# Optimization experiments

Measured on AMD Instinct MI355X. Metric: run time of the kernel, lower is better.

## Reference

```python
import jax, jax.numpy as jnp
import numpy as np

B, N, C, W = 64, 4096, 128, 64
WIN = N - W + 1  # 4033, length of each sliding-filter input
BN_EPS = 1e-5


def setup_inputs() -> dict:
    key = jax.random.key(0)
    ks = jax.random.split(key, 8)
    s_in = 1.0 / np.sqrt(WIN)   # nn.Linear default init scale
    s_2 = 1.0 / np.sqrt(2.0)
    s_out = 1.0 / np.sqrt(W)
    return {
        "x": jax.random.normal(ks[0], (B, N, C, 2), dtype=jnp.float32),
        "w_in_real": jax.random.normal(ks[1], (C, WIN), dtype=jnp.float32) * s_in,
        "w_in_imag": jax.random.normal(ks[2], (C, WIN), dtype=jnp.float32) * s_in,
        "A_nonlin": jax.random.normal(ks[3], (C, 2, 2), dtype=jnp.float32) * s_2,
        "Wc": jax.random.normal(ks[4], (2, 2), dtype=jnp.float32) * s_2,
        "w_out_real": jax.random.normal(ks[5], (C, W), dtype=jnp.float32) * s_out,
        "w_out_imag": jax.random.normal(ks[6], (C, W), dtype=jnp.float32) * s_out,
        "bn_gamma": jnp.ones((C,), dtype=jnp.float32),
        "bn_beta": jnp.zeros((C,), dtype=jnp.float32),
    }


def _depthwise_corr(sig, w):
    # sig: [B, N, C], w: [C, K] -> [B, N-K+1, C]
    # filtered[b, t, c] = sum_k sig[b, t+k, c] * w[c, k]  (matches per-channel Linear on slices)
    rhs = w.T[:, None, :]  # [K, 1, C]
    return jax.lax.conv_general_dilated(
        sig, rhs, window_strides=(1,), padding="VALID",
        dimension_numbers=("NWC", "WIO", "NWC"),
        feature_group_count=sig.shape[-1])


def reference(x, w_in_real, w_in_imag, A_nonlin, Wc, w_out_real, w_out_imag, bn_gamma, bn_beta):
    xr, xi = x[..., 0], x[..., 1]               # [B, N, C]
    # --- per-channel sliding input filters (out_window positions) ---
    fr = _depthwise_corr(xr, w_in_real)          # [B, W, C]
    fi = _depthwise_corr(xi, w_in_imag)          # [B, W, C]
    v = jnp.stack([fr, fi], axis=-1)             # [B, W, C, 2]
    # --- per-channel 2x2 linear: out_j = sum_i A[c, j, i] * v_i ---
    u = jnp.einsum("bwci,cji->bwcj", v, A_nonlin)
    amp = jnp.sum(u * u, axis=-1, keepdims=True)  # r^2 + i^2
    u = amp * u
    # --- shared 2x2 coeff linear ---
    u = jnp.einsum("bwci,ji->bwcj", u, Wc)
    # --- per-channel output filters over the out_window axis ---
    out_r = jnp.einsum("bwc,cw->bc", u[..., 0], w_out_real)
    out_i = jnp.einsum("bwc,cw->bc", u[..., 1], w_out_imag)
    out = jnp.stack([out_r, out_i], axis=-1)     # [B, C, 2]
    # --- BatchNorm1d(C), training-mode batch statistics over (B, last) dims ---
    mean = jnp.mean(out, axis=(0, 2), keepdims=True)
    var = jnp.mean((out - mean) ** 2, axis=(0, 2), keepdims=True)
    out = (out - mean) * jax.lax.rsqrt(var + BN_EPS)
    return out * bn_gamma[None, :, None] + bn_beta[None, :, None]
```

## Files before the change

kernel.cpp:

```cpp
#include <hip/hip_runtime.h>

typedef float v2f __attribute__((ext_vector_type(2)));
typedef float v4f __attribute__((ext_vector_type(4)));

#define B_ 64
#define N_ 4096
#define C_ 128
#define W_ 64
#define WIN_ 4033
#define CG 16
#define NCHUNK 256
#define KPAD 4176
#define WSTRIDE 338

__global__ void prep_w(const float* __restrict__ wr, const float* __restrict__ wi,
                       v2f* __restrict__ w2pad) {
  int idx = blockIdx.x * 256 + threadIdx.x;
  int c = idx / KPAD;
  int kk = idx - c * KPAD;
  int k = kk - 64;
  v2f v = {0.f, 0.f};
  if (k >= 0 && k < WIN_) {
    v.x = wr[c * WIN_ + k];
    v.y = wi[c * WIN_ + k];
  }
  w2pad[idx] = v;
}

__global__ __launch_bounds__(256, 2) void conv_main(
    const v2f* __restrict__ x2,
    const v2f* __restrict__ w2pad,
    const float* __restrict__ Anl,
    const float* __restrict__ Wcm,
    const float* __restrict__ wor,
    const float* __restrict__ woi,
    float* __restrict__ pre) {
  __shared__ __attribute__((aligned(16))) v2f wsh[CG * WSTRIDE];

  int tid = threadIdx.x;
  int bb = blockIdx.x >> 3;
  int cg = blockIdx.x & 7;
  int cbase = cg * CG;
  int cl = (tid >> 2) & 15;
  int t0g = tid & 3;
  int np = tid >> 6;
  int t0 = t0g << 4;
  int nbase = np << 6;

  v2f zero = {0.f, 0.f};
  v2f acc[16];
#pragma unroll
  for (int i = 0; i < 16; i++) acc[i] = zero;

  const v2f* xg = x2 + (size_t)bb * N_ * C_ + cbase + cl;
  const v2f* wrow = wsh + cl * WSTRIDE;

  for (int n0 = 0; n0 < N_; n0 += NCHUNK) {
    {
      const v4f* wsrc = (const v4f*)(w2pad + (size_t)cbase * KPAD + n0);
      v4f* wdst = (v4f*)wsh;
      for (int i = tid; i < CG * 168; i += 256) {
        int c = i / 168;
        int u = i - c * 168;
        wdst[c * 169 + u] = wsrc[(size_t)c * (KPAD / 2) + u];
      }
    }
    __syncthreads();

    v2f wA[16], wB[16], xA[16], xB[16];
#pragma unroll
    for (int m = 0; m < 16; m++) wA[m] = wrow[nbase + 48 - t0 + m];
#pragma unroll
    for (int j = 0; j < 16; j++) xA[j] = xg[(size_t)(n0 + nbase + j) * C_];

    auto pref = [&](int nb, v2f* xv) {
#pragma unroll
      for (int j = 0; j < 16; j++) xv[j] = xg[(size_t)(n0 + nb + j) * C_];
    };
    auto do16 = [&](int nb, const v2f* xv, const v2f* wold, v2f* wnew) {
#pragma unroll
      for (int j = 0; j < 16; j++) wnew[j] = wrow[nb + 64 - t0 + j];
#pragma unroll
      for (int j = 0; j < 16; j++) {
#pragma unroll
        for (int i = 0; i < 16; i++) {
          int e = j - i;
          v2f wv = (e < 0) ? wold[16 + e] : wnew[e];
          acc[i] = __builtin_elementwise_fma(xv[j], wv, acc[i]);
        }
      }
    };

    pref(nbase + 16, xB);
    do16(nbase + 0, xA, wA, wB);
    pref(nbase + 32, xA);
    do16(nbase + 16, xB, wB, wA);
    pref(nbase + 48, xB);
    do16(nbase + 32, xA, wA, wB);
    do16(nbase + 48, xB, wB, wA);
    __syncthreads();
  }

  v2f* fpart = wsh;
#pragma unroll
  for (int i = 0; i < 16; i++) fpart[((np * CG + cl) << 6) + t0 + i] = acc[i];
  __syncthreads();

  int cl2 = tid & 15;
  int tq = tid >> 4;
  int c = cbase + cl2;
  float a00 = Anl[c * 4 + 0], a01 = Anl[c * 4 + 1];
  float a10 = Anl[c * 4 + 2], a11 = Anl[c * 4 + 3];
  float wc00 = Wcm[0], wc01 = Wcm[1], wc10 = Wcm[2], wc11 = Wcm[3];
  float or_ = 0.f, oi_ = 0.f;
#pragma unroll
  for (int q = 0; q < 4; q++) {
    int t = tq + (q << 4);
    v2f f = fpart[(0 * CG + cl2) * 64 + t] + fpart[(1 * CG + cl2) * 64 + t] +
            fpart[(2 * CG + cl2) * 64 + t] + fpart[(3 * CG + cl2) * 64 + t];
    float ur = a00 * f.x + a01 * f.y;
    float ui = a10 * f.x + a11 * f.y;
    float amp = ur * ur + ui * ui;
    ur *= amp;
    ui *= amp;
    float vr = wc00 * ur + wc01 * ui;
    float vi = wc10 * ur + wc11 * ui;
    or_ += vr * wor[c * 64 + t];
    oi_ += vi * woi[c * 64 + t];
  }
  or_ += __shfl_down(or_, 16, 64);
  oi_ += __shfl_down(oi_, 16, 64);
  or_ += __shfl_down(or_, 32, 64);
  oi_ += __shfl_down(oi_, 32, 64);
  __syncthreads();
  v2f* opart = wsh;
  if ((tid & 63) < 16) {
    v2f t = {or_, oi_};
    opart[(tid >> 6) * 16 + cl2] = t;
  }
  __syncthreads();
  if (tid < 16) {
    v2f r = opart[cl2] + opart[16 + cl2] + opart[32 + cl2] + opart[48 + cl2];
    pre[((size_t)bb * C_ + cbase + cl2) * 2 + 0] = r.x;
    pre[((size_t)bb * C_ + cbase + cl2) * 2 + 1] = r.y;
  }
}

__global__ void bn_kernel(const float* __restrict__ pre, const float* __restrict__ gamma,
                          const float* __restrict__ beta, float* __restrict__ out) {
  int c = blockIdx.x, tid = threadIdx.x;
  int b = tid >> 1, comp = tid & 1;
  float v = pre[((size_t)b * C_ + c) * 2 + comp];
  float s = v, s2 = v * v;
#pragma unroll
  for (int d = 32; d > 0; d >>= 1) {
    s += __shfl_down(s, d, 64);
    s2 += __shfl_down(s2, d, 64);
  }
  __shared__ float red[4];
  if ((tid & 63) == 0) {
    red[(tid >> 6) * 2 + 0] = s;
    red[(tid >> 6) * 2 + 1] = s2;
  }
  __syncthreads();
  float sum = red[0] + red[2], sumsq = red[1] + red[3];
  float mean = sum * 0.0078125f;
  float var = sumsq * 0.0078125f - mean * mean;
  float inv = rsqrtf(var + 1e-5f);
  out[((size_t)b * C_ + c) * 2 + comp] = (v - mean) * inv * gamma[c] + beta[c];
}

extern "C" void kernel_launch(void* const* d_in, const int* in_sizes, int n_in,
                              void* d_out, int out_size, void* d_ws, size_t ws_size,
                              hipStream_t stream) {
  (void)in_sizes; (void)n_in; (void)out_size; (void)ws_size;
  const float* x   = (const float*)d_in[0];
  const float* wir = (const float*)d_in[1];
  const float* wii = (const float*)d_in[2];
  const float* Anl = (const float*)d_in[3];
  const float* Wcm = (const float*)d_in[4];
  const float* wrr = (const float*)d_in[5];
  const float* wri = (const float*)d_in[6];
  const float* gam = (const float*)d_in[7];
  const float* bet = (const float*)d_in[8];

  v2f* w2pad = (v2f*)d_ws;
  float* pre = (float*)((char*)d_ws + (size_t)C_ * KPAD * sizeof(v2f));

  prep_w<<<(C_ * KPAD) / 256, 256, 0, stream>>>(wir, wii, w2pad);
  conv_main<<<B_ * (C_ / CG), 256, 0, stream>>>((const v2f*)x, w2pad, Anl, Wcm,
                                                wrr, wri, pre);
  bn_kernel<<<C_, 128, 0, stream>>>(pre, gam, bet, (float*)d_out);
}
```

Measured before the change: 495.1 us.

## Split sequence across blocks with atomic reduction, larger register tiles, inline weight staging

Reworks the sliding-filter kernel. Each thread now holds 32 output positions instead of 16 and uses a register window that shifts by 8, so each shared-memory weight load feeds more FMAs. Each block covers two batches, and the sequence is split into two halves handled by separate blocks whose partial sums are combined with global atomics into a zeroed buffer. The padded-weight prep kernel is removed and weights are staged straight from the inputs into skewed shared memory to avoid bank conflicts. The nonlinearity and output filter move into their own kernel. The cost is a memset, many atomics, an extra launch, and higher register pressure from the 32-accumulator tile.

New measurement: 936.6 us. 89.2% more time.

```diff
diff --git a/kernel.cpp b/kernel.cpp
--- a/kernel.cpp
+++ b/kernel.cpp
@@ -1,7 +1,6 @@
 #include <hip/hip_runtime.h>
 
 typedef float v2f __attribute__((ext_vector_type(2)));
-typedef float v4f __attribute__((ext_vector_type(4)));
 
 #define B_ 64
 #define N_ 4096
@@ -9,140 +8,153 @@
 #define W_ 64
 #define WIN_ 4033
 #define CG 16
-#define NCHUNK 256
-#define KPAD 4176
-#define WSTRIDE 338
-
-__global__ void prep_w(const float* __restrict__ wr, const float* __restrict__ wi,
-                       v2f* __restrict__ w2pad) {
-  int idx = blockIdx.x * 256 + threadIdx.x;
-  int c = idx / KPAD;
-  int kk = idx - c * KPAD;
-  int k = kk - 64;
-  v2f v = {0.f, 0.f};
-  if (k >= 0 && k < WIN_) {
-    v.x = wr[c * WIN_ + k];
-    v.y = wi[c * WIN_ + k];
-  }
-  w2pad[idx] = v;
-}
+#define CHUNK 256
+#define STAGE 336
+#define SROW 357
+#define NH 2
+#define HALF_N 2048
+
+__device__ __forceinline__ int skew(int u) { return u + (u >> 4); }
 
 __global__ __launch_bounds__(256, 2) void conv_main(
     const v2f* __restrict__ x2,
-    const v2f* __restrict__ w2pad,
-    const float* __restrict__ Anl,
-    const float* __restrict__ Wcm,
-    const float* __restrict__ wor,
-    const float* __restrict__ woi,
-    float* __restrict__ pre) {
-  __shared__ __attribute__((aligned(16))) v2f wsh[CG * WSTRIDE];
+    const float* __restrict__ wr,
+    const float* __restrict__ wi,
+    float* __restrict__ facc) {
+  __shared__ __attribute__((aligned(16))) v2f wsh[CG * SROW];
 
   int tid = threadIdx.x;
-  int bb = blockIdx.x >> 3;
-  int cg = blockIdx.x & 7;
+  int bid = blockIdx.x;
+  int half = bid & 1;
+  int cg = (bid >> 1) & 7;
+  int bp = bid >> 4;
+  int cl = tid & 15;
+  int tg = (tid >> 4) & 1;
+  int np = (tid >> 5) & 3;
+  int bsel = tid >> 7;
+  int b = bp * 2 + bsel;
   int cbase = cg * CG;
-  int cl = (tid >> 2) & 15;
-  int t0g = tid & 3;
-  int np = tid >> 6;
-  int t0 = t0g << 4;
-  int nbase = np << 6;
-
-  v2f zero = {0.f, 0.f};
-  v2f acc[16];
-#pragma unroll
-  for (int i = 0; i < 16; i++) acc[i] = zero;
-
-  const v2f* xg = x2 + (size_t)bb * N_ * C_ + cbase + cl;
-  const v2f* wrow = wsh + cl * WSTRIDE;
-
-  for (int n0 = 0; n0 < N_; n0 += NCHUNK) {
-    {
-      const v4f* wsrc = (const v4f*)(w2pad + (size_t)cbase * KPAD + n0);
-      v4f* wdst = (v4f*)wsh;
-      for (int i = tid; i < CG * 168; i += 256) {
-        int c = i / 168;
-        int u = i - c * 168;
-        wdst[c * 169 + u] = wsrc[(size_t)c * (KPAD / 2) + u];
+  int c = cbase + cl;
+  int t0 = tg * 32;
+  int halfstart = half * HALF_N;
+  int nthr = np * 64;
+
+  v2f acc[32];
+#pragma unroll
+  for (int i = 0; i < 32; i++) acc[i] = (v2f){0.f, 0.f};
+
+  const v2f* xg = x2 + ((size_t)b * N_ + halfstart) * C_ + c;
+  const v2f* wrow = wsh + cl * SROW;
+
+  v2f win[40];
+  v2f xw[3][8];
+
+  for (int ch = 0; ch < 8; ++ch) {
+    int n0 = halfstart + ch * CHUNK;
+    int ncb = ch * CHUNK + nthr;
+
+#pragma unroll
+    for (int j = 0; j < 8; j++) xw[0][j] = xg[(size_t)(ncb + j) * C_];
+#pragma unroll
+    for (int j = 0; j < 8; j++) xw[1][j] = xg[(size_t)(ncb + 8 + j) * C_];
+
+    __syncthreads();
+
+#pragma unroll
+    for (int cc = 0; cc < CG; ++cc) {
+      const float* wrp = wr + (size_t)(cbase + cc) * WIN_;
+      const float* wip = wi + (size_t)(cbase + cc) * WIN_;
+      {
+        int u = tid;
+        int k = n0 + u - 64;
+        bool ok = (unsigned)k < (unsigned)WIN_;
+        v2f v;
+        v.x = ok ? wrp[k] : 0.f;
+        v.y = ok ? wip[k] : 0.f;
+        wsh[cc * SROW + skew(u)] = v;
+      }
+      if (tid < STAGE - 256) {
+        int u = tid + 256;
+        int k = n0 + u - 64;
+        bool ok = (unsigned)k < (unsigned)WIN_;
+        v2f v;
+        v.x = ok ? wrp[k] : 0.f;
+        v.y = ok ? wip[k] : 0.f;
+        wsh[cc * SROW + skew(u)] = v;
       }
     }
     __syncthreads();
 
-    v2f wA[16], wB[16], xA[16], xB[16];
-#pragma unroll
-    for (int m = 0; m < 16; m++) wA[m] = wrow[nbase + 48 - t0 + m];
-#pragma unroll
-    for (int j = 0; j < 16; j++) xA[j] = xg[(size_t)(n0 + nbase + j) * C_];
-
-    auto pref = [&](int nb, v2f* xv) {
-#pragma unroll
-      for (int j = 0; j < 16; j++) xv[j] = xg[(size_t)(n0 + nb + j) * C_];
-    };
-    auto do16 = [&](int nb, const v2f* xv, const v2f* wold, v2f* wnew) {
-#pragma unroll
-      for (int j = 0; j < 16; j++) wnew[j] = wrow[nb + 64 - t0 + j];
-#pragma unroll
-      for (int j = 0; j < 16; j++) {
-#pragma unroll
-        for (int i = 0; i < 16; i++) {
-          int e = j - i;
-          v2f wv = (e < 0) ? wold[16 + e] : wnew[e];
-          acc[i] = __builtin_elementwise_fma(xv[j], wv, acc[i]);
+#pragma unroll
+    for (int m = 0; m < 40; m++) win[m] = wrow[skew(nthr + 33 - t0 + m)];
+
+#pragma unroll
+    for (int blk = 0; blk < 8; ++blk) {
+      int nbc = nthr + blk * 8;
+      if (blk < 6) {
+#pragma unroll
+        for (int j = 0; j < 8; j++)
+          xw[(blk + 2) % 3][j] = xg[(size_t)(ch * CHUNK + nbc + 16 + j) * C_];
+      }
+      const v2f* xv = xw[blk % 3];
+#pragma unroll
+      for (int j = 0; j < 8; j++) {
+#pragma unroll
+        for (int i = 0; i < 32; i++) {
+          acc[i] = __builtin_elementwise_fma(xv[j], win[31 + j - i], acc[i]);
         }
       }
-    };
-
-    pref(nbase + 16, xB);
-    do16(nbase + 0, xA, wA, wB);
-    pref(nbase + 32, xA);
-    do16(nbase + 16, xB, wB, wA);
-    pref(nbase + 48, xB);
-    do16(nbase + 32, xA, wA, wB);
-    do16(nbase + 48, xB, wB, wA);
-    __syncthreads();
-  }
-
-  v2f* fpart = wsh;
-#pragma unroll
-  for (int i = 0; i < 16; i++) fpart[((np * CG + cl) << 6) + t0 + i] = acc[i];
-  __syncthreads();
-
-  int cl2 = tid & 15;
-  int tq = tid >> 4;
-  int c = cbase + cl2;
+      if (blk < 7) {
+#pragma unroll
+        for (int m = 0; m < 32; m++) win[m] = win[m + 8];
+#pragma unroll
+        for (int r = 0; r < 8; r++)
+          win[32 + r] = wrow[skew(nbc + 73 - t0 + r)];
+      }
+    }
+  }
+
+  float* fp = facc + (((size_t)b * C_ + c) * 64 + t0) * 2;
+#pragma unroll
+  for (int i = 0; i < 32; i++) {
+    atomicAdd(fp + 2 * i + 0, acc[i].x);
+    atomicAdd(fp + 2 * i + 1, acc[i].y);
+  }
+}
+
+__global__ void nonlin_out(const float* __restrict__ faccf,
+                           const float* __restrict__ Anl,
+                           const float* __restrict__ Wcm,
+                           const float* __restrict__ wor,
+                           const float* __restrict__ woi,
+                           float* __restrict__ pre) {
+  int tid = threadIdx.x;
+  int p = tid >> 6;
+  int t = tid & 63;
+  int idx = blockIdx.x * 4 + p;
+  int b = idx >> 7;
+  int c = idx & 127;
+  const v2f* f2 = (const v2f*)faccf;
+  v2f f = f2[((size_t)b * C_ + c) * 64 + t];
   float a00 = Anl[c * 4 + 0], a01 = Anl[c * 4 + 1];
   float a10 = Anl[c * 4 + 2], a11 = Anl[c * 4 + 3];
-  float wc00 = Wcm[0], wc01 = Wcm[1], wc10 = Wcm[2], wc11 = Wcm[3];
-  float or_ = 0.f, oi_ = 0.f;
-#pragma unroll
-  for (int q = 0; q < 4; q++) {
-    int t = tq + (q << 4);
-    v2f f = fpart[(0 * CG + cl2) * 64 + t] + fpart[(1 * CG + cl2) * 64 + t] +
-            fpart[(2 * CG + cl2) * 64 + t] + fpart[(3 * CG + cl2) * 64 + t];
-    float ur = a00 * f.x + a01 * f.y;
-    float ui = a10 * f.x + a11 * f.y;
-    float amp = ur * ur + ui * ui;
-    ur *= amp;
-    ui *= amp;
-    float vr = wc00 * ur + wc01 * ui;
-    float vi = wc10 * ur + wc11 * ui;
-    or_ += vr * wor[c * 64 + t];
-    oi_ += vi * woi[c * 64 + t];
-  }
-  or_ += __shfl_down(or_, 16, 64);
-  oi_ += __shfl_down(oi_, 16, 64);
-  or_ += __shfl_down(or_, 32, 64);
-  oi_ += __shfl_down(oi_, 32, 64);
-  __syncthreads();
-  v2f* opart = wsh;
-  if ((tid & 63) < 16) {
-    v2f t = {or_, oi_};
-    opart[(tid >> 6) * 16 + cl2] = t;
-  }
-  __syncthreads();
-  if (tid < 16) {
-    v2f r = opart[cl2] + opart[16 + cl2] + opart[32 + cl2] + opart[48 + cl2];
-    pre[((size_t)bb * C_ + cbase + cl2) * 2 + 0] = r.x;
-    pre[((size_t)bb * C_ + cbase + cl2) * 2 + 1] = r.y;
+  float ur = a00 * f.x + a01 * f.y;
+  float ui = a10 * f.x + a11 * f.y;
+  float amp = ur * ur + ui * ui;
+  ur *= amp;
+  ui *= amp;
+  float vr = Wcm[0] * ur + Wcm[1] * ui;
+  float vi = Wcm[2] * ur + Wcm[3] * ui;
+  float or_ = vr * wor[c * 64 + t];
+  float oi_ = vi * woi[c * 64 + t];
+#pragma unroll
+  for (int d = 32; d > 0; d >>= 1) {
+    or_ += __shfl_down(or_, d, 64);
+    oi_ += __shfl_down(oi_, d, 64);
+  }
+  if (t == 0) {
+    pre[((size_t)b * C_ + c) * 2 + 0] = or_;
+    pre[((size_t)b * C_ + c) * 2 + 1] = oi_;
   }
 }
 
@@ -184,11 +196,11 @@
   const float* gam = (const float*)d_in[7];
   const float* bet = (const float*)d_in[8];
 
-  v2f* w2pad = (v2f*)d_ws;
-  float* pre = (float*)((char*)d_ws + (size_t)C_ * KPAD * sizeof(v2f));
-
-  prep_w<<<(C_ * KPAD) / 256, 256, 0, stream>>>(wir, wii, w2pad);
-  conv_main<<<B_ * (C_ / CG), 256, 0, stream>>>((const v2f*)x, w2pad, Anl, Wcm,
-                                                wrr, wri, pre);
+  float* facc = (float*)d_ws;
+  float* pre  = facc + (size_t)B_ * C_ * 64 * 2;
+
+  hipMemsetAsync(facc, 0, (size_t)B_ * C_ * 64 * 2 * sizeof(float), stream);
+  conv_main<<<32 * 8 * NH, 256, 0, stream>>>((const v2f*)x, wir, wii, facc);
+  nonlin_out<<<(B_ * C_) / 4, 256, 0, stream>>>(facc, Anl, Wcm, wrr, wri, pre);
   bn_kernel<<<C_, 128, 0, stream>>>(pre, gam, bet, (float*)d_out);
 }
```

## Shrink per-thread tile to 8x8, halve channel group, use packed FMA asm

Applied to the files above, without the earlier changes.

The conv kernel is restructured so each thread computes 8 output positions over 8-sample input blocks with a sliding 16-entry weight register window, instead of 16x16 tiles. Channel groups shrink from 16 to 8, which doubles the grid, and launch bounds rise to 4 blocks per CU to cut register pressure and raise occupancy. The x loads for the next chunk are issued before the weight staging sync, and the FMAs use inline v_pk_fma_f32. The cost is less register reuse per x/w load, more LDS traffic per FMA, and scalar (non-vector) weight staging copies.

Measured after the change: 550.3 us. +11.2%, slower.

```diff
diff --git a/kernel.cpp b/kernel.cpp
--- a/kernel.cpp
+++ b/kernel.cpp
@@ -1,17 +1,23 @@
 #include <hip/hip_runtime.h>
 
 typedef float v2f __attribute__((ext_vector_type(2)));
-typedef float v4f __attribute__((ext_vector_type(4)));
 
 #define B_ 64
 #define N_ 4096
 #define C_ 128
 #define W_ 64
 #define WIN_ 4033
-#define CG 16
-#define NCHUNK 256
+#define CG 8
+#define CHUNK 256
+#define STAGE 336
+#define SROW 337
 #define KPAD 4176
-#define WSTRIDE 338
+
+__device__ __forceinline__ v2f pk_fma(v2f a, v2f b, v2f c) {
+  v2f d;
+  asm("v_pk_fma_f32 %0, %1, %2, %3" : "=v"(d) : "v"(a), "v"(b), "v"(c));
+  return d;
+}
 
 __global__ void prep_w(const float* __restrict__ wr, const float* __restrict__ wi,
                        v2f* __restrict__ w2pad) {
@@ -27,7 +33,7 @@
   w2pad[idx] = v;
 }
 
-__global__ __launch_bounds__(256, 2) void conv_main(
+__global__ __launch_bounds__(256, 4) void conv_main(
     const v2f* __restrict__ x2,
     const v2f* __restrict__ w2pad,
     const float* __restrict__ Anl,
@@ -35,89 +41,87 @@
     const float* __restrict__ wor,
     const float* __restrict__ woi,
     float* __restrict__ pre) {
-  __shared__ __attribute__((aligned(16))) v2f wsh[CG * WSTRIDE];
+  __shared__ __attribute__((aligned(16))) v2f wsh[CG * SROW];
 
   int tid = threadIdx.x;
-  int bb = blockIdx.x >> 3;
-  int cg = blockIdx.x & 7;
+  int bid = blockIdx.x;
+  int bb = bid >> 4;
+  int cg = bid & 15;
   int cbase = cg * CG;
-  int cl = (tid >> 2) & 15;
-  int t0g = tid & 3;
+  int cl = tid & 7;
+  int tg = (tid >> 3) & 7;
   int np = tid >> 6;
-  int t0 = t0g << 4;
+  int t0 = tg << 3;
   int nbase = np << 6;
 
-  v2f zero = {0.f, 0.f};
-  v2f acc[16];
+  v2f acc[8];
 #pragma unroll
-  for (int i = 0; i < 16; i++) acc[i] = zero;
+  for (int i = 0; i < 8; i++) acc[i] = (v2f){0.f, 0.f};
 
   const v2f* xg = x2 + (size_t)bb * N_ * C_ + cbase + cl;
-  const v2f* wrow = wsh + cl * WSTRIDE;
+  const v2f* wrow = wsh + cl * SROW;
+  const v2f* wsrc = w2pad + (size_t)cbase * KPAD;
 
-  for (int n0 = 0; n0 < N_; n0 += NCHUNK) {
-    {
-      const v4f* wsrc = (const v4f*)(w2pad + (size_t)cbase * KPAD + n0);
-      v4f* wdst = (v4f*)wsh;
-      for (int i = tid; i < CG * 168; i += 256) {
-        int c = i / 168;
-        int u = i - c * 168;
-        wdst[c * 169 + u] = wsrc[(size_t)c * (KPAD / 2) + u];
-      }
+  v2f W[16], xA[8], xB[8];
+
+  for (int n0 = 0; n0 < N_; n0 += CHUNK) {
+#pragma unroll
+    for (int j = 0; j < 8; j++) xA[j] = xg[(size_t)(n0 + nbase + j) * C_];
+
+    __syncthreads();
+    for (int i = tid; i < CG * STAGE; i += 256) {
+      int c = i / STAGE;
+      int u = i - c * STAGE;
+      wsh[c * SROW + u] = wsrc[(size_t)c * KPAD + n0 + u];
     }
     __syncthreads();
 
-    v2f wA[16], wB[16], xA[16], xB[16];
 #pragma unroll
-    for (int m = 0; m < 16; m++) wA[m] = wrow[nbase + 48 - t0 + m];
+    for (int m = 0; m < 16; m++) W[m] = wrow[nbase + 57 - t0 + m];
+
 #pragma unroll
-    for (int j = 0; j < 16; j++) xA[j] = xg[(size_t)(n0 + nbase + j) * C_];
-
-    auto pref = [&](int nb, v2f* xv) {
+    for (int blk = 0; blk < 8; ++blk) {
+      int nb = nbase + blk * 8;
+      const v2f* xv = (blk & 1) ? xB : xA;
+      v2f* xo = (blk & 1) ? xA : xB;
+      if (blk < 7) {
 #pragma unroll
-      for (int j = 0; j < 16; j++) xv[j] = xg[(size_t)(n0 + nb + j) * C_];
-    };
-    auto do16 = [&](int nb, const v2f* xv, const v2f* wold, v2f* wnew) {
+        for (int j = 0; j < 8; j++) xo[j] = xg[(size_t)(n0 + nb + 8 + j) * C_];
+      }
 #pragma unroll
-      for (int j = 0; j < 16; j++) wnew[j] = wrow[nb + 64 - t0 + j];
+      for (int j = 0; j < 8; j++) {
 #pragma unroll
-      for (int j = 0; j < 16; j++) {
-#pragma unroll
-        for (int i = 0; i < 16; i++) {
-          int e = j - i;
-          v2f wv = (e < 0) ? wold[16 + e] : wnew[e];
-          acc[i] = __builtin_elementwise_fma(xv[j], wv, acc[i]);
+        for (int i = 0; i < 8; i++) {
+          acc[i] = pk_fma(xv[j], W[7 + j - i], acc[i]);
         }
       }
-    };
-
-    pref(nbase + 16, xB);
-    do16(nbase + 0, xA, wA, wB);
-    pref(nbase + 32, xA);
-    do16(nbase + 16, xB, wB, wA);
-    pref(nbase + 48, xB);
-    do16(nbase + 32, xA, wA, wB);
-    do16(nbase + 48, xB, wB, wA);
-    __syncthreads();
+      if (blk < 7) {
+#pragma unroll
+        for (int m = 0; m < 8; m++) W[m] = W[m + 8];
+#pragma unroll
+        for (int r = 0; r < 8; r++) W[8 + r] = wrow[nb + 73 - t0 + r];
+      }
+    }
   }
 
+  __syncthreads();
   v2f* fpart = wsh;
 #pragma unroll
-  for (int i = 0; i < 16; i++) fpart[((np * CG + cl) << 6) + t0 + i] = acc[i];
+  for (int i = 0; i < 8; i++) fpart[(np * 8 + cl) * 65 + t0 + i] = acc[i];
   __syncthreads();
 
-  int cl2 = tid & 15;
-  int tq = tid >> 4;
+  int cl2 = tid & 7;
+  int tt = tid >> 3;
   int c = cbase + cl2;
   float a00 = Anl[c * 4 + 0], a01 = Anl[c * 4 + 1];
   float a10 = Anl[c * 4 + 2], a11 = Anl[c * 4 + 3];
   float wc00 = Wcm[0], wc01 = Wcm[1], wc10 = Wcm[2], wc11 = Wcm[3];
   float or_ = 0.f, oi_ = 0.f;
 #pragma unroll
-  for (int q = 0; q < 4; q++) {
-    int t = tq + (q << 4);
-    v2f f = fpart[(0 * CG + cl2) * 64 + t] + fpart[(1 * CG + cl2) * 64 + t] +
-            fpart[(2 * CG + cl2) * 64 + t] + fpart[(3 * CG + cl2) * 64 + t];
+  for (int h = 0; h < 2; h++) {
+    int t = tt + (h << 5);
+    v2f f = fpart[(0 * 8 + cl2) * 65 + t] + fpart[(1 * 8 + cl2) * 65 + t] +
+            fpart[(2 * 8 + cl2) * 65 + t] + fpart[(3 * 8 + cl2) * 65 + t];
     float ur = a00 * f.x + a01 * f.y;
     float ui = a10 * f.x + a11 * f.y;
     float amp = ur * ur + ui * ui;
@@ -128,21 +132,18 @@
     or_ += vr * wor[c * 64 + t];
     oi_ += vi * woi[c * 64 + t];
   }
+  or_ += __shfl_down(or_, 32, 64);
+  oi_ += __shfl_down(oi_, 32, 64);
   or_ += __shfl_down(or_, 16, 64);
   oi_ += __shfl_down(oi_, 16, 64);
-  or_ += __shfl_down(or_, 32, 64);
-  oi_ += __shfl_down(oi_, 32, 64);
+  or_ += __shfl_down(or_, 8, 64);
+  oi_ += __shfl_down(oi_, 8, 64);
+  v2f* opart = wsh + 2200;
+  if ((tid & 63) < 8) opart[(tid >> 6) * 8 + cl2] = (v2f){or_, oi_};
   __syncthreads();
-  v2f* opart = wsh;
-  if ((tid & 63) < 16) {
-    v2f t = {or_, oi_};
-    opart[(tid >> 6) * 16 + cl2] = t;
-  }
-  __syncthreads();
-  if (tid < 16) {
-    v2f r = opart[cl2] + opart[16 + cl2] + opart[32 + cl2] + opart[48 + cl2];
-    pre[((size_t)bb * C_ + cbase + cl2) * 2 + 0] = r.x;
-    pre[((size_t)bb * C_ + cbase + cl2) * 2 + 1] = r.y;
+  if (tid < 8) {
+    v2f r = opart[cl2] + opart[8 + cl2] + opart[16 + cl2] + opart[24 + cl2];
+    ((v2f*)pre)[(size_t)bb * C_ + cbase + cl2] = r;
   }
 }
 
```
